# Performance work log

Measured on AMD Instinct MI355X. Metric: run time of the kernel, lower is better.

The kernel has to match this reference:

```python
import jax, jax.numpy as jnp
import numpy as np

B, S, D, H = 2, 2048, 1024, 16
Dh = D // H

def setup_inputs() -> dict:
    key = jax.random.key(0)
    ks = jax.random.split(key, 11)
    def lin(k, fan_in):
        bound = 1.0 / np.sqrt(fan_in)
        kw, kb = jax.random.split(k)
        W = jax.random.uniform(kw, (D, D), jnp.float32, -bound, bound)
        b = jax.random.uniform(kb, (D,), jnp.float32, -bound, bound)
        return W, b
    Wq, bq = lin(ks[0], D)
    Wk, bk = lin(ks[1], D)
    Wv, bv = lin(ks[2], D)
    Wo, bo = lin(ks[3], D)
    Q = jax.random.normal(ks[4], (B, S, D), jnp.float32)
    K = jax.random.normal(ks[5], (B, S, D), jnp.float32)
    V = jax.random.normal(ks[6], (B, S, D), jnp.float32)
    return {"Q": Q, "K": K, "V": V, "Wq": Wq, "bq": bq, "Wk": Wk, "bk": bk,
            "Wv": Wv, "bv": bv, "Wo": Wo, "bo": bo}

def _split_heads(x):
    # [B,S,D] -> [B,H,S,Dh]
    b, s, _ = x.shape
    return x.reshape(b, s, H, Dh).transpose(0, 2, 1, 3)

def reference(Q, K, V, Wq, bq, Wk, bk, Wv, bv, Wo, bo):
    q = _split_heads(Q @ Wq.T + bq)
    k = _split_heads(K @ Wk.T + bk)
    v = _split_heads(V @ Wv.T + bv)
    scores = jnp.einsum('bhqd,bhkd->bhqk', q, k) / jnp.sqrt(jnp.float32(Dh))
    attn = jax.nn.softmax(scores, axis=-1)
    out = jnp.einsum('bhqk,bhkd->bhqd', attn, v)  # [B,H,S,Dh]
    out = out.transpose(0, 2, 1, 3).reshape(Q.shape[0], Q.shape[1], D)
    return out @ Wo.T + bo
```

## Files before the change

### kernel.cpp

```cpp
#include <hip/hip_runtime.h>

#define SEQ 2048
#define DMODEL 1024
#define NH 16
#define DH 64

typedef __attribute__((ext_vector_type(8))) short bf16x8;
typedef __attribute__((ext_vector_type(4))) short bf16x4;
typedef __attribute__((ext_vector_type(4))) float floatx4;
typedef __attribute__((ext_vector_type(4))) unsigned short u16x4;
typedef unsigned short u16;
typedef unsigned int u32;

typedef const void __attribute__((address_space(1)))* as1cvp;
typedef void __attribute__((address_space(3)))* as3vp;

__device__ __forceinline__ void glds16(const void* g, void* l) {
    __builtin_amdgcn_global_load_lds((as1cvp)g, (as3vp)l, 16, 0, 0);
}

__device__ __forceinline__ u16 f2bf(float f) {
    union { u32 u; float f; } v; v.f = f;
    return (u16)((v.u + 0x8000u) >> 16);
}

__device__ __forceinline__ u32 pk2(float a, float b) {
    union { u32 u; float f; } x, y; x.f = a; y.f = b;
    u32 xr = x.u + 0x8000u, yr = y.u + 0x8000u;
#if __has_builtin(__builtin_amdgcn_perm)
    return __builtin_amdgcn_perm(yr, xr, 0x07060302u);
#else
    return (xr >> 16) | (yr & 0xffff0000u);
#endif
}

__device__ __forceinline__ float ex2(float x) {
#if __has_builtin(__builtin_amdgcn_exp2f)
    return __builtin_amdgcn_exp2f(x);
#else
    float r; asm("v_exp_f32 %0, %1" : "=v"(r) : "v"(x)); return r;
#endif
}

__device__ __forceinline__ floatx4 mfma16(bf16x4 a, bf16x4 b, floatx4 c) {
#if __has_builtin(__builtin_amdgcn_mfma_f32_16x16x16bf16_1k)
    return __builtin_amdgcn_mfma_f32_16x16x16bf16_1k(a, b, c, 0, 0, 0);
#else
    asm volatile("v_mfma_f32_16x16x16_bf16 %0, %1, %2, %0" : "+v"(c) : "v"(a), "v"(b));
    return c;
#endif
}

__device__ __forceinline__ uint4 cvt8(const float* __restrict__ p) {
    float4 a = *(const float4*)p;
    float4 b = *(const float4*)(p + 4);
    uint4 q;
    q.x = pk2(a.x, a.y); q.y = pk2(a.z, a.w);
    q.z = pk2(b.x, b.y); q.w = pk2(b.z, b.w);
    return q;
}

#define QSCALE 0.18033688011112042f

__global__ __launch_bounds__(256) void cvt_all(
    const float* __restrict__ Q, const float* __restrict__ K, const float* __restrict__ V,
    const float* __restrict__ W0, const float* __restrict__ W1,
    const float* __restrict__ W2, const float* __restrict__ W3,
    u16* __restrict__ Qb, u16* __restrict__ Kb, u16* __restrict__ Vb,
    u16* __restrict__ Wb)
{
    const int y = blockIdx.y;
    const float* src; u16* dst;
    if (y == 0)      { src = Q;  dst = Qb; }
    else if (y == 1) { src = K;  dst = Kb; }
    else if (y == 2) { src = V;  dst = Vb; }
    else {
        if (blockIdx.x >= 512) return;
        src = (y == 3) ? W0 : (y == 4) ? W1 : (y == 5) ? W2 : W3;
        dst = Wb + (size_t)(y - 3) * 1048576;
    }
    size_t i = ((size_t)blockIdx.x * 256 + threadIdx.x) * 8;
    *(uint4*)(dst + i) = cvt8(src + i);
}

__global__ __launch_bounds__(256) void cvt_w(
    const float* __restrict__ W0, const float* __restrict__ W1,
    const float* __restrict__ W2, const float* __restrict__ W3,
    u16* __restrict__ out)
{
    const float* src = (blockIdx.y == 0) ? W0 : (blockIdx.y == 1) ? W1
                     : (blockIdx.y == 2) ? W2 : W3;
    size_t i = ((size_t)blockIdx.x * 256 + threadIdx.x) * 8;
    *(uint4*)(out + (size_t)blockIdx.y * 1048576 + i) = cvt8(src + i);
}

__device__ __forceinline__ void qkv_store(
    int z, u16* __restrict__ outp, int rowg, int col, floatx4 a4, float bv, float sc)
{
    union { u32 w[2]; u16 h[4]; u16x4 v4; } pk;
    pk.w[0] = pk2((a4[0] + bv) * sc, (a4[1] + bv) * sc);
    pk.w[1] = pk2((a4[2] + bv) * sc, (a4[3] + bv) * sc);
    int b = rowg >> 11, s = rowg & 2047, h = col >> 6, d = col & 63;
    if (z < 2) {
#pragma unroll
        for (int r = 0; r < 4; r++)
            outp[((size_t)(b * NH + h) * SEQ + s + r) * DH + d] = pk.h[r];
    } else {
        *(u16x4*)(outp + ((size_t)(b * NH + h) * DH + d) * SEQ + s) = pk.v4;
    }
}

__global__ __launch_bounds__(256) void gemm_qkv_bb(
    const u16* __restrict__ Qb, const u16* __restrict__ Kb, const u16* __restrict__ Vb,
    const u16* __restrict__ Wb,
    const float* __restrict__ b0, const float* __restrict__ b1, const float* __restrict__ b2,
    u16* __restrict__ qo, u16* __restrict__ ko, u16* __restrict__ vto)
{
    __shared__ __align__(16) u16 As[3][4096];
    __shared__ __align__(16) u16 Bs[3][4096];
    const int tid = threadIdx.x, l = tid & 63, w = tid >> 6;
    const int lm = l & 15, quad = l >> 4;
    const int wr = (w >> 1) * 64, wc = (w & 1) * 64;
    const int bm = blockIdx.y * 128, bn = blockIdx.x * 128;
    const int z = blockIdx.z;
    const u16* A      = (z == 0) ? Qb : (z == 1) ? Kb : Vb;
    const u16* W      = Wb + (size_t)z * 1048576;
    const float* bias = (z == 0) ? b0 : (z == 1) ? b1 : b2;

    const int srow = tid >> 2, scol = (tid & 3) * 8;

    floatx4 acc[4][4];
#pragma unroll
    for (int i = 0; i < 4; i++)
#pragma unroll
        for (int j = 0; j < 4; j++) acc[i][j] = (floatx4){0.f, 0.f, 0.f, 0.f};

#define QKV_STAGE(I, NB) do { \
        const int kt_ = (I) * 32; \
        glds16(A + (size_t)(bm + srow) * DMODEL + kt_ + scol, As[NB] + w * 512); \
        glds16(A + (size_t)(bm + 64 + srow) * DMODEL + kt_ + scol, As[NB] + 2048 + w * 512); \
        glds16(W + (size_t)(bn + srow) * DMODEL + kt_ + scol, Bs[NB] + w * 512); \
        glds16(W + (size_t)(bn + 64 + srow) * DMODEL + kt_ + scol, Bs[NB] + 2048 + w * 512); \
    } while (0)

    QKV_STAGE(0, 0);
    QKV_STAGE(1, 1);
    asm volatile("s_waitcnt vmcnt(4)" ::: "memory");
    __builtin_amdgcn_s_barrier();

    int cur = 0, nx = 2;
    for (int i = 0; i < 32; i++) {
        bf16x8 af[4], bfr[4];
#pragma unroll
        for (int mi = 0; mi < 4; mi++)
            af[mi] = *(const bf16x8*)(As[cur] + (wr + mi * 16 + lm) * 32 + quad * 8);
#pragma unroll
        for (int ni = 0; ni < 4; ni++)
            bfr[ni] = *(const bf16x8*)(Bs[cur] + (wc + ni * 16 + lm) * 32 + quad * 8);
#pragma unroll
        for (int mi = 0; mi < 4; mi++)
#pragma unroll
            for (int ni = 0; ni < 4; ni++)
                acc[mi][ni] = __builtin_amdgcn_mfma_f32_16x16x32_bf16(
                    af[mi], bfr[ni], acc[mi][ni], 0, 0, 0);

        if (i + 2 < 32) {
            QKV_STAGE(i + 2, nx);
            asm volatile("s_waitcnt vmcnt(4)" ::: "memory");
            __builtin_amdgcn_s_barrier();
        } else if (i + 1 < 32) {
            asm volatile("s_waitcnt vmcnt(0)" ::: "memory");
            __builtin_amdgcn_s_barrier();
        }
        cur = (cur == 2) ? 0 : cur + 1;
        nx  = (nx == 2) ? 0 : nx + 1;
    }
#undef QKV_STAGE

    const float sc = (z == 0) ? QSCALE : 1.0f;
    u16* outp = (z == 0) ? qo : (z == 1) ? ko : vto;
#pragma unroll
    for (int ni = 0; ni < 4; ni++) {
        int col = bn + wc + ni * 16 + lm;
        float bv = bias[col];
#pragma unroll
        for (int mi = 0; mi < 4; mi++)
            qkv_store(z, outp, bm + wr + mi * 16 + quad * 4, col, acc[mi][ni], bv, sc);
    }
}

template<bool WBF>
__global__ __launch_bounds__(256) void gemm_qkv(
    const float* __restrict__ Qf, const float* __restrict__ Kf, const float* __restrict__ Vf,
    const void* __restrict__ W0, const void* __restrict__ W1, const void* __restrict__ W2,
    const float* __restrict__ b0, const float* __restrict__ b1, const float* __restrict__ b2,
    u16* __restrict__ qo, u16* __restrict__ ko, u16* __restrict__ vto)
{
    __shared__ __align__(16) u16 As[128 * 32];
    __shared__ __align__(16) u16 Bs[128 * 32];
    const int tid = threadIdx.x, l = tid & 63, w = tid >> 6;
    const int lm = l & 15, quad = l >> 4;
    const int wr = (w >> 1) * 64, wc = (w & 1) * 64;
    const int bm = blockIdx.y * 128, bn = blockIdx.x * 128;
    const int z = blockIdx.z;
    const float* A    = (z == 0) ? Qf : (z == 1) ? Kf : Vf;
    const void* Wp    = (z == 0) ? W0 : (z == 1) ? W1 : W2;
    const float* bias = (z == 0) ? b0 : (z == 1) ? b1 : b2;

    floatx4 acc[4][4];
#pragma unroll
    for (int i = 0; i < 4; i++)
#pragma unroll
        for (int j = 0; j < 4; j++) acc[i][j] = (floatx4){0.f, 0.f, 0.f, 0.f};

    for (int kt = 0; kt < DMODEL; kt += 32) {
        __syncthreads();
#pragma unroll
        for (int j = 0; j < 2; j++) {
            int ch = j * 256 + tid, row = ch >> 2, c = ch & 3;
            *(uint4*)(As + ch * 8) = cvt8(A + (size_t)(bm + row) * DMODEL + kt + c * 8);
        }
        if (WBF) {
            const u16* Wc = (const u16*)Wp;
            glds16(Wc + (size_t)(bn + (tid >> 2)) * DMODEL + kt + (tid & 3) * 8, Bs + w * 512);
            glds16(Wc + (size_t)(bn + 64 + (tid >> 2)) * DMODEL + kt + (tid & 3) * 8, Bs + 2048 + w * 512);
        } else {
            const float* Wf = (const float*)Wp;
#pragma unroll
            for (int j = 0; j < 2; j++) {
                int ch = j * 256 + tid, row = ch >> 2, c = ch & 3;
                *(uint4*)(Bs + ch * 8) = cvt8(Wf + (size_t)(bn + row) * DMODEL + kt + c * 8);
            }
        }
        __syncthreads();

        bf16x8 af[4], bfr[4];
#pragma unroll
        for (int mi = 0; mi < 4; mi++)
            af[mi] = *(const bf16x8*)(As + (wr + mi * 16 + lm) * 32 + quad * 8);
#pragma unroll
        for (int ni = 0; ni < 4; ni++)
            bfr[ni] = *(const bf16x8*)(Bs + (wc + ni * 16 + lm) * 32 + quad * 8);
#pragma unroll
        for (int mi = 0; mi < 4; mi++)
#pragma unroll
            for (int ni = 0; ni < 4; ni++)
                acc[mi][ni] = __builtin_amdgcn_mfma_f32_16x16x32_bf16(
                    af[mi], bfr[ni], acc[mi][ni], 0, 0, 0);
    }

    const float sc = (z == 0) ? QSCALE : 1.0f;
    u16* outp = (z == 0) ? qo : (z == 1) ? ko : vto;
#pragma unroll
    for (int ni = 0; ni < 4; ni++) {
        int col = bn + wc + ni * 16 + lm;
        float bv = bias[col];
#pragma unroll
        for (int mi = 0; mi < 4; mi++)
            qkv_store(z, outp, bm + wr + mi * 16 + quad * 4, col, acc[mi][ni], bv, sc);
    }
}

__global__ __launch_bounds__(256) void gemm_o_p(
    const u16* __restrict__ A, const u16* __restrict__ W,
    const float* __restrict__ bias, float* __restrict__ out)
{
    __shared__ __align__(16) u16 As[3][4096];
    __shared__ __align__(16) u16 Bs[3][2048];
    const int tid = threadIdx.x, l = tid & 63, w = tid >> 6;
    const int lm = l & 15, quad = l >> 4;
    const int bm = blockIdx.y * 128, bn = blockIdx.x * 64;

    floatx4 acc[2][4];
#pragma unroll
    for (int i = 0; i < 2; i++)
#pragma unroll
        for (int j = 0; j < 4; j++) acc[i][j] = (floatx4){0.f, 0.f, 0.f, 0.f};

#define O_STAGE(I, NB) do { \
        const int kt_ = (I) * 32; \
        glds16(A + (size_t)(bm + (tid >> 2)) * DMODEL + kt_ + (tid & 3) * 8, As[NB] + w * 512); \
        glds16(A + (size_t)(bm + 64 + (tid >> 2)) * DMODEL + kt_ + (tid & 3) * 8, As[NB] + 2048 + w * 512); \
        glds16(W + (size_t)(bn + (tid >> 2)) * DMODEL + kt_ + (tid & 3) * 8, Bs[NB] + w * 512); \
    } while (0)

    O_STAGE(0, 0);
    O_STAGE(1, 1);
    asm volatile("s_waitcnt vmcnt(3)" ::: "memory");
    __builtin_amdgcn_s_barrier();

    int cur = 0, nx = 2;
    for (int i = 0; i < 32; i++) {
        bf16x8 af[2], bfr[4];
#pragma unroll
        for (int mi = 0; mi < 2; mi++)
            af[mi] = *(const bf16x8*)(As[cur] + (w * 32 + mi * 16 + lm) * 32 + quad * 8);
#pragma unroll
        for (int ni = 0; ni < 4; ni++)
            bfr[ni] = *(const bf16x8*)(Bs[cur] + (ni * 16 + lm) * 32 + quad * 8);
#pragma unroll
        for (int mi = 0; mi < 2; mi++)
#pragma unroll
            for (int ni = 0; ni < 4; ni++)
                acc[mi][ni] = __builtin_amdgcn_mfma_f32_16x16x32_bf16(
                    af[mi], bfr[ni], acc[mi][ni], 0, 0, 0);

        if (i + 2 < 32) {
            O_STAGE(i + 2, nx);
            asm volatile("s_waitcnt vmcnt(3)" ::: "memory");
            __builtin_amdgcn_s_barrier();
        } else if (i + 1 < 32) {
            asm volatile("s_waitcnt vmcnt(0)" ::: "memory");
            __builtin_amdgcn_s_barrier();
        }
        cur = (cur == 2) ? 0 : cur + 1;
        nx  = (nx == 2) ? 0 : nx + 1;
    }
#undef O_STAGE

#pragma unroll
    for (int ni = 0; ni < 4; ni++) {
        int col = bn + ni * 16 + lm;
        float bv = bias[col];
#pragma unroll
        for (int mi = 0; mi < 2; mi++) {
#pragma unroll
            for (int r = 0; r < 4; r++) {
                int rowg = bm + w * 32 + mi * 16 + quad * 4 + r;
                out[(size_t)rowg * DMODEL + col] = acc[mi][ni][r] + bv;
            }
        }
    }
}

template<bool WBF>
__global__ __launch_bounds__(256) void gemm_o(
    const u16* __restrict__ A, const void* __restrict__ Wp,
    const float* __restrict__ bias, float* __restrict__ out)
{
    __shared__ __align__(16) u16 As[128 * 32];
    __shared__ __align__(16) u16 Bs[64 * 32];
    const int tid = threadIdx.x, l = tid & 63, w = tid >> 6;
    const int lm = l & 15, quad = l >> 4;
    const int bm = blockIdx.y * 128, bn = blockIdx.x * 64;

    floatx4 acc[2][4];
#pragma unroll
    for (int i = 0; i < 2; i++)
#pragma unroll
        for (int j = 0; j < 4; j++) acc[i][j] = (floatx4){0.f, 0.f, 0.f, 0.f};

    for (int kt = 0; kt < DMODEL; kt += 32) {
        __syncthreads();
        glds16(A + (size_t)(bm + (tid >> 2)) * DMODEL + kt + (tid & 3) * 8, As + w * 512);
        glds16(A + (size_t)(bm + 64 + (tid >> 2)) * DMODEL + kt + (tid & 3) * 8, As + 2048 + w * 512);
        if (WBF) {
            glds16((const u16*)Wp + (size_t)(bn + (tid >> 2)) * DMODEL + kt + (tid & 3) * 8, Bs + w * 512);
        } else {
            *(uint4*)(Bs + tid * 8) =
                cvt8((const float*)Wp + (size_t)(bn + (tid >> 2)) * DMODEL + kt + (tid & 3) * 8);
        }
        __syncthreads();

        bf16x8 af[2], bfr[4];
#pragma unroll
        for (int mi = 0; mi < 2; mi++)
            af[mi] = *(const bf16x8*)(As + (w * 32 + mi * 16 + lm) * 32 + quad * 8);
#pragma unroll
        for (int ni = 0; ni < 4; ni++)
            bfr[ni] = *(const bf16x8*)(Bs + (ni * 16 + lm) * 32 + quad * 8);
#pragma unroll
        for (int mi = 0; mi < 2; mi++)
#pragma unroll
            for (int ni = 0; ni < 4; ni++)
                acc[mi][ni] = __builtin_amdgcn_mfma_f32_16x16x32_bf16(
                    af[mi], bfr[ni], acc[mi][ni], 0, 0, 0);
    }

#pragma unroll
    for (int ni = 0; ni < 4; ni++) {
        int col = bn + ni * 16 + lm;
        float bv = bias[col];
#pragma unroll
        for (int mi = 0; mi < 2; mi++) {
#pragma unroll
            for (int r = 0; r < 4; r++) {
                int rowg = bm + w * 32 + mi * 16 + quad * 4 + r;
                out[(size_t)rowg * DMODEL + col] = acc[mi][ni][r] + bv;
            }
        }
    }
}

#define SP 72
#define TS (64 * SP)
#define BUFSZ (4 * TS)
__global__ __launch_bounds__(256, 2) void attn_kernel(
    const u16* __restrict__ q, const u16* __restrict__ k,
    const u16* __restrict__ vt, u16* __restrict__ out)
{
    __shared__ __align__(16) u16 smem[2 * BUFSZ];
    const int tid = threadIdx.x, l = tid & 63, w = tid >> 6;
    const int lm = l & 15, quad = l >> 4;
    const int qt = blockIdx.x, bh = blockIdx.y;
    const int b = bh >> 4, h = bh & 15;
    const int rg = w & 1, half = w >> 1;

    bf16x8 qf[4][2];
#pragma unroll
    for (int nt = 0; nt < 4; nt++) {
        int row = qt * 128 + rg * 64 + nt * 16 + lm;
        const u16* qp = q + ((size_t)bh * SEQ + row) * DH;
        qf[nt][0] = *(const bf16x8*)(qp + quad * 8);
        qf[nt][1] = *(const bf16x8*)(qp + 32 + quad * 8);
    }

    floatx4 O[4][4];
#pragma unroll
    for (int dt = 0; dt < 4; dt++)
#pragma unroll
        for (int nt = 0; nt < 4; nt++) O[dt][nt] = (floatx4){0.f, 0.f, 0.f, 0.f};
    floatx4 Ol[4];
#pragma unroll
    for (int nt = 0; nt < 4; nt++) Ol[nt] = (floatx4){0.f, 0.f, 0.f, 0.f};

    const bf16x4 onesb = {(short)0x3F80, (short)0x3F80, (short)0x3F80, (short)0x3F80};

    const int srow = tid >> 2, sc4 = tid & 3;
    const u16* kbase = k + (size_t)bh * SEQ * DH;
    const u16* vbase = vt + (size_t)bh * DH * SEQ;

    uint4 kA0, kA1, kB0, kB1, vA0, vA1, vB0, vB1;
#define LOADT(T) do { \
        const u16* kgA = kbase + (size_t)((T) * 64 + srow) * DH + sc4 * 16; \
        const u16* kgB = kbase + (size_t)(1024 + (T) * 64 + srow) * DH + sc4 * 16; \
        kA0 = *(const uint4*)kgA;       kA1 = *(const uint4*)(kgA + 8); \
        kB0 = *(const uint4*)kgB;       kB1 = *(const uint4*)(kgB + 8); \
        const u16* vgA = vbase + (size_t)srow * SEQ + (T) * 64 + sc4 * 16; \
        const u16* vgB = vgA + 1024; \
        vA0 = *(const uint4*)vgA;       vA1 = *(const uint4*)(vgA + 8); \
        vB0 = *(const uint4*)vgB;       vB1 = *(const uint4*)(vgB + 8); \
    } while (0)
#define WRBUF(BUF) do { \
        u16* K0 = smem + (BUF) * BUFSZ; \
        u16* K1 = K0 + TS; \
        u16* V0 = K0 + 2 * TS; \
        u16* V1 = K0 + 3 * TS; \
        *(uint4*)(K0 + srow * SP + sc4 * 16)     = kA0; \
        *(uint4*)(K0 + srow * SP + sc4 * 16 + 8) = kA1; \
        *(uint4*)(K1 + srow * SP + sc4 * 16)     = kB0; \
        *(uint4*)(K1 + srow * SP + sc4 * 16 + 8) = kB1; \
        *(uint2*)(V0 + srow * SP + 0 * 16 + sc4 * 4) = make_uint2(vA0.x, vA0.y); \
        *(uint2*)(V0 + srow * SP + 1 * 16 + sc4 * 4) = make_uint2(vA0.z, vA0.w); \
        *(uint2*)(V0 + srow * SP + 2 * 16 + sc4 * 4) = make_uint2(vA1.x, vA1.y); \
        *(uint2*)(V0 + srow * SP + 3 * 16 + sc4 * 4) = make_uint2(vA1.z, vA1.w); \
        *(uint2*)(V1 + srow * SP + 0 * 16 + sc4 * 4) = make_uint2(vB0.x, vB0.y); \
        *(uint2*)(V1 + srow * SP + 1 * 16 + sc4 * 4) = make_uint2(vB0.z, vB0.w); \
        *(uint2*)(V1 + srow * SP + 2 * 16 + sc4 * 4) = make_uint2(vB1.x, vB1.y); \
        *(uint2*)(V1 + srow * SP + 3 * 16 + sc4 * 4) = make_uint2(vB1.z, vB1.w); \
    } while (0)

    LOADT(0);
    WRBUF(0);
    LOADT(1);
    asm volatile("s_waitcnt lgkmcnt(0)" ::: "memory");
    __builtin_amdgcn_s_barrier();

    for (int t = 0; t < 16; t++) {
        const int cur = t & 1;
        const u16* Kh = smem + cur * BUFSZ + half * TS;
        const u16* Vh = smem + cur * BUFSZ + (2 + half) * TS;

        floatx4 Sc[4][4];
        __builtin_amdgcn_s_setprio(1);
#pragma unroll
        for (int mt = 0; mt < 4; mt++) {
            bf16x8 ka0 = *(const bf16x8*)(Kh + (mt * 16 + lm) * SP + quad * 8);
            bf16x8 ka1 = *(const bf16x8*)(Kh + (mt * 16 + lm) * SP + 32 + quad * 8);
#pragma unroll
            for (int nt = 0; nt < 4; nt++) {
                floatx4 c = (floatx4){0.f, 0.f, 0.f, 0.f};
                c = __builtin_amdgcn_mfma_f32_16x16x32_bf16(ka0, qf[nt][0], c, 0, 0, 0);
                c = __builtin_amdgcn_mfma_f32_16x16x32_bf16(ka1, qf[nt][1], c, 0, 0, 0);
                Sc[mt][nt] = c;
            }
        }
        __builtin_amdgcn_s_setprio(0);

        if (t + 1 < 16) {
            asm volatile("s_waitcnt vmcnt(0)" ::: "memory");
            WRBUF(cur ^ 1);
            if (t + 2 < 16) LOADT(t + 2);
        }

        bf16x4 pb[4][4];
#pragma unroll
        for (int mt = 0; mt < 4; mt++) {
#pragma unroll
            for (int nt = 0; nt < 4; nt++) {
#pragma unroll
                for (int r = 0; r < 4; r++) Sc[mt][nt][r] = ex2(Sc[mt][nt][r]);
                union { u32 w2[2]; bf16x4 v; } pku;
                pku.w2[0] = pk2(Sc[mt][nt][0], Sc[mt][nt][1]);
                pku.w2[1] = pk2(Sc[mt][nt][2], Sc[mt][nt][3]);
                pb[mt][nt] = pku.v;
            }
        }

        __builtin_amdgcn_s_setprio(1);
#pragma unroll
        for (int nt = 0; nt < 4; nt++) {
            Ol[nt] = mfma16(onesb, pb[0][nt], Ol[nt]);
            Ol[nt] = mfma16(onesb, pb[1][nt], Ol[nt]);
            Ol[nt] = mfma16(onesb, pb[2][nt], Ol[nt]);
            Ol[nt] = mfma16(onesb, pb[3][nt], Ol[nt]);
        }

#pragma unroll
        for (int dt = 0; dt < 4; dt++) {
            const u16* vp = Vh + (dt * 16 + lm) * SP + quad * 16;
            bf16x8 v8a = *(const bf16x8*)vp;
            bf16x8 v8b = *(const bf16x8*)(vp + 8);
            bf16x4 va0 = __builtin_shufflevector(v8a, v8a, 0, 1, 2, 3);
            bf16x4 va1 = __builtin_shufflevector(v8a, v8a, 4, 5, 6, 7);
            bf16x4 va2 = __builtin_shufflevector(v8b, v8b, 0, 1, 2, 3);
            bf16x4 va3 = __builtin_shufflevector(v8b, v8b, 4, 5, 6, 7);
#pragma unroll
            for (int nt = 0; nt < 4; nt++) {
                O[dt][nt] = mfma16(va0, pb[0][nt], O[dt][nt]);
                O[dt][nt] = mfma16(va1, pb[1][nt], O[dt][nt]);
                O[dt][nt] = mfma16(va2, pb[2][nt], O[dt][nt]);
                O[dt][nt] = mfma16(va3, pb[3][nt], O[dt][nt]);
            }
        }
        __builtin_amdgcn_s_setprio(0);

        asm volatile("s_waitcnt lgkmcnt(0)" ::: "memory");
        __builtin_amdgcn_s_barrier();
    }
#undef LOADT
#undef WRBUF

    float* obuf  = (float*)smem;
    float* mlbuf = (float*)smem + 8704;
    if (w >= 2) {
        float* ob = obuf + (rg * 64 + l) * 68;
        float* ml = mlbuf + (rg * 64 + l) * 5;
#pragma unroll
        for (int nt = 0; nt < 4; nt++) {
#pragma unroll
            for (int dt = 0; dt < 4; dt++)
                *(floatx4*)(ob + nt * 16 + dt * 4) = O[dt][nt];
            ml[nt] = Ol[nt][0];
        }
    }
    __syncthreads();
    if (w < 2) {
        float* ob = obuf + (rg * 64 + l) * 68;
        float* ml = mlbuf + (rg * 64 + l) * 5;
#pragma unroll
        for (int nt = 0; nt < 4; nt++) {
            float lB = ml[nt];
            float inv = 1.0f / (Ol[nt][0] + lB);
            int s = qt * 128 + rg * 64 + nt * 16 + lm;
            u16* op = out + ((size_t)b * SEQ + s) * DMODEL + h * DH;
#pragma unroll
            for (int dt = 0; dt < 4; dt++) {
                floatx4 Ob = *(const floatx4*)(ob + nt * 16 + dt * 4);
                union { u32 w2[2]; u16x4 v; } pku;
                pku.w2[0] = pk2((O[dt][nt][0] + Ob[0]) * inv,
                                (O[dt][nt][1] + Ob[1]) * inv);
                pku.w2[1] = pk2((O[dt][nt][2] + Ob[2]) * inv,
                                (O[dt][nt][3] + Ob[3]) * inv);
                *(u16x4*)(op + dt * 16 + quad * 4) = pku.v;
            }
        }
    }
}

extern "C" void kernel_launch(void* const* d_in, const int* in_sizes, int n_in,
                              void* d_out, int out_size, void* d_ws, size_t ws_size,
                              hipStream_t stream) {
    (void)in_sizes; (void)n_in; (void)out_size;
    const float* Q  = (const float*)d_in[0];
    const float* K  = (const float*)d_in[1];
    const float* V  = (const float*)d_in[2];
    const float* Wq = (const float*)d_in[3];
    const float* bq = (const float*)d_in[4];
    const float* Wk = (const float*)d_in[5];
    const float* bk = (const float*)d_in[6];
    const float* Wv = (const float*)d_in[7];
    const float* bv = (const float*)d_in[8];
    const float* Wo = (const float*)d_in[9];
    const float* bo = (const float*)d_in[10];

    const size_t NEL = (size_t)2 * NH * SEQ * DH;
    u16* base = (u16*)d_ws;
    dim3 bb(256);
    dim3 ab(256);

    if (ws_size >= 8 * NEL * 2) {
        u16* Qb   = base;
        u16* Kb   = Qb + NEL;
        u16* Vb   = Kb + NEL;
        u16* Wb   = Vb + NEL;
        u16* qws  = Wb + NEL;
        u16* kws  = qws + NEL;
        u16* vtws = kws + NEL;
        u16* aws  = vtws + NEL;
        cvt_all<<<dim3(2048, 7), bb, 0, stream>>>(Q, K, V, Wq, Wk, Wv, Wo, Qb, Kb, Vb, Wb);
        gemm_qkv_bb<<<dim3(8, 32, 3), bb, 0, stream>>>(
            Qb, Kb, Vb, Wb, bq, bk, bv, qws, kws, vtws);
        attn_kernel<<<dim3(SEQ / 128, 2 * NH), ab, 0, stream>>>(qws, kws, vtws, aws);
        gemm_o_p<<<dim3(16, 32), bb, 0, stream>>>(aws, Wb + 3145728, bo, (float*)d_out);
    } else if (ws_size >= 5 * NEL * 2) {
        u16* Wb = base;
        u16* qws = base + NEL; u16* kws = qws + NEL; u16* vtws = kws + NEL; u16* aws = vtws + NEL;
        cvt_w<<<dim3(512, 4), bb, 0, stream>>>(Wq, Wk, Wv, Wo, Wb);
        gemm_qkv<true><<<dim3(8, 32, 3), bb, 0, stream>>>(
            Q, K, V, Wb, Wb + 1048576, Wb + 2097152, bq, bk, bv, qws, kws, vtws);
        attn_kernel<<<dim3(SEQ / 128, 2 * NH), ab, 0, stream>>>(qws, kws, vtws, aws);
        gemm_o_p<<<dim3(16, 32), bb, 0, stream>>>(aws, Wb + 3145728, bo, (float*)d_out);
    } else {
        u16* qws = base; u16* kws = qws + NEL; u16* vtws = kws + NEL; u16* aws = vtws + NEL;
        gemm_qkv<false><<<dim3(8, 32, 3), bb, 0, stream>>>(
            Q, K, V, Wq, Wk, Wv, bq, bk, bv, qws, kws, vtws);
        attn_kernel<<<dim3(SEQ / 128, 2 * NH), ab, 0, stream>>>(qws, kws, vtws, aws);
        gemm_o<false><<<dim3(16, 32), bb, 0, stream>>>(aws, Wo, bo, (float*)d_out);
    }
}
```

Measured before the change: 220.8 us.

## Use 16x16x32 bf16 MFMA for PV and row-sum via permuted K layout

Replaces the 16x16x16 MFMAs in the P·V and row-sum accumulation with 16x16x32 MFMAs, halving the instruction count. K rows are stored to LDS under a permutation so that two adjacent score tiles pack into one 8-wide bf16 operand that lines up with contiguous V columns. V stores become plain 16-byte writes and its fragment loads no longer need splitting. Correctness depends on the row permutation exactly matching the MFMA k-index ordering.

New measurement: 218.7 us. No clear change (-0.9%).

```diff
diff --git a/kernel.cpp b/kernel.cpp
--- a/kernel.cpp
+++ b/kernel.cpp
@@ -42,13 +42,8 @@
 #endif
 }
 
-__device__ __forceinline__ floatx4 mfma16(bf16x4 a, bf16x4 b, floatx4 c) {
-#if __has_builtin(__builtin_amdgcn_mfma_f32_16x16x16bf16_1k)
-    return __builtin_amdgcn_mfma_f32_16x16x16bf16_1k(a, b, c, 0, 0, 0);
-#else
-    asm volatile("v_mfma_f32_16x16x16_bf16 %0, %1, %2, %0" : "+v"(c) : "v"(a), "v"(b));
-    return c;
-#endif
+__device__ __forceinline__ floatx4 mfma32(bf16x8 a, bf16x8 b, floatx4 c) {
+    return __builtin_amdgcn_mfma_f32_16x16x32_bf16(a, b, c, 0, 0, 0);
 }
 
 __device__ __forceinline__ uint4 cvt8(const float* __restrict__ p) {
@@ -424,9 +419,11 @@
 #pragma unroll
     for (int nt = 0; nt < 4; nt++) Ol[nt] = (floatx4){0.f, 0.f, 0.f, 0.f};
 
-    const bf16x4 onesb = {(short)0x3F80, (short)0x3F80, (short)0x3F80, (short)0x3F80};
+    const bf16x8 ones8 = {(short)0x3F80, (short)0x3F80, (short)0x3F80, (short)0x3F80,
+                          (short)0x3F80, (short)0x3F80, (short)0x3F80, (short)0x3F80};
 
     const int srow = tid >> 2, sc4 = tid & 3;
+    const int prow = (srow & 32) | ((srow & 4) << 2) | ((srow & 24) >> 1) | (srow & 3);
     const u16* kbase = k + (size_t)bh * SEQ * DH;
     const u16* vbase = vt + (size_t)bh * DH * SEQ;
 
@@ -446,18 +443,14 @@
         u16* K1 = K0 + TS; \
         u16* V0 = K0 + 2 * TS; \
         u16* V1 = K0 + 3 * TS; \
-        *(uint4*)(K0 + srow * SP + sc4 * 16)     = kA0; \
-        *(uint4*)(K0 + srow * SP + sc4 * 16 + 8) = kA1; \
-        *(uint4*)(K1 + srow * SP + sc4 * 16)     = kB0; \
-        *(uint4*)(K1 + srow * SP + sc4 * 16 + 8) = kB1; \
-        *(uint2*)(V0 + srow * SP + 0 * 16 + sc4 * 4) = make_uint2(vA0.x, vA0.y); \
-        *(uint2*)(V0 + srow * SP + 1 * 16 + sc4 * 4) = make_uint2(vA0.z, vA0.w); \
-        *(uint2*)(V0 + srow * SP + 2 * 16 + sc4 * 4) = make_uint2(vA1.x, vA1.y); \
-        *(uint2*)(V0 + srow * SP + 3 * 16 + sc4 * 4) = make_uint2(vA1.z, vA1.w); \
-        *(uint2*)(V1 + srow * SP + 0 * 16 + sc4 * 4) = make_uint2(vB0.x, vB0.y); \
-        *(uint2*)(V1 + srow * SP + 1 * 16 + sc4 * 4) = make_uint2(vB0.z, vB0.w); \
-        *(uint2*)(V1 + srow * SP + 2 * 16 + sc4 * 4) = make_uint2(vB1.x, vB1.y); \
-        *(uint2*)(V1 + srow * SP + 3 * 16 + sc4 * 4) = make_uint2(vB1.z, vB1.w); \
+        *(uint4*)(K0 + prow * SP + sc4 * 16)     = kA0; \
+        *(uint4*)(K0 + prow * SP + sc4 * 16 + 8) = kA1; \
+        *(uint4*)(K1 + prow * SP + sc4 * 16)     = kB0; \
+        *(uint4*)(K1 + prow * SP + sc4 * 16 + 8) = kB1; \
+        *(uint4*)(V0 + srow * SP + sc4 * 16)     = vA0; \
+        *(uint4*)(V0 + srow * SP + sc4 * 16 + 8) = vA1; \
+        *(uint4*)(V1 + srow * SP + sc4 * 16)     = vB0; \
+        *(uint4*)(V1 + srow * SP + sc4 * 16 + 8) = vB1; \
     } while (0)
 
     LOADT(0);
@@ -474,15 +467,15 @@
         floatx4 Sc[4][4];
         __builtin_amdgcn_s_setprio(1);
 #pragma unroll
-        for (int mt = 0; mt < 4; mt++) {
-            bf16x8 ka0 = *(const bf16x8*)(Kh + (mt * 16 + lm) * SP + quad * 8);
-            bf16x8 ka1 = *(const bf16x8*)(Kh + (mt * 16 + lm) * SP + 32 + quad * 8);
+        for (int sub = 0; sub < 4; sub++) {
+            bf16x8 ka0 = *(const bf16x8*)(Kh + (sub * 16 + lm) * SP + quad * 8);
+            bf16x8 ka1 = *(const bf16x8*)(Kh + (sub * 16 + lm) * SP + 32 + quad * 8);
 #pragma unroll
             for (int nt = 0; nt < 4; nt++) {
                 floatx4 c = (floatx4){0.f, 0.f, 0.f, 0.f};
-                c = __builtin_amdgcn_mfma_f32_16x16x32_bf16(ka0, qf[nt][0], c, 0, 0, 0);
-                c = __builtin_amdgcn_mfma_f32_16x16x32_bf16(ka1, qf[nt][1], c, 0, 0, 0);
-                Sc[mt][nt] = c;
+                c = mfma32(ka0, qf[nt][0], c);
+                c = mfma32(ka1, qf[nt][1], c);
+                Sc[sub][nt] = c;
             }
         }
         __builtin_amdgcn_s_setprio(0);
@@ -493,44 +486,37 @@
             if (t + 2 < 16) LOADT(t + 2);
         }
 
-        bf16x4 pb[4][4];
-#pragma unroll
-        for (int mt = 0; mt < 4; mt++) {
+        bf16x8 pbm[2][4];
+#pragma unroll
+        for (int p = 0; p < 2; p++)
 #pragma unroll
             for (int nt = 0; nt < 4; nt++) {
-#pragma unroll
-                for (int r = 0; r < 4; r++) Sc[mt][nt][r] = ex2(Sc[mt][nt][r]);
-                union { u32 w2[2]; bf16x4 v; } pku;
-                pku.w2[0] = pk2(Sc[mt][nt][0], Sc[mt][nt][1]);
-                pku.w2[1] = pk2(Sc[mt][nt][2], Sc[mt][nt][3]);
-                pb[mt][nt] = pku.v;
+                floatx4 sa = Sc[p * 2][nt], sb = Sc[p * 2 + 1][nt];
+#pragma unroll
+                for (int r = 0; r < 4; r++) { sa[r] = ex2(sa[r]); sb[r] = ex2(sb[r]); }
+                union { u32 w4[4]; bf16x8 v; } pku;
+                pku.w4[0] = pk2(sa[0], sa[1]);
+                pku.w4[1] = pk2(sa[2], sa[3]);
+                pku.w4[2] = pk2(sb[0], sb[1]);
+                pku.w4[3] = pk2(sb[2], sb[3]);
+                pbm[p][nt] = pku.v;
             }
-        }
 
         __builtin_amdgcn_s_setprio(1);
 #pragma unroll
         for (int nt = 0; nt < 4; nt++) {
-            Ol[nt] = mfma16(onesb, pb[0][nt], Ol[nt]);
-            Ol[nt] = mfma16(onesb, pb[1][nt], Ol[nt]);
-            Ol[nt] = mfma16(onesb, pb[2][nt], Ol[nt]);
-            Ol[nt] = mfma16(onesb, pb[3][nt], Ol[nt]);
+            Ol[nt] = mfma32(ones8, pbm[0][nt], Ol[nt]);
+            Ol[nt] = mfma32(ones8, pbm[1][nt], Ol[nt]);
         }
 
 #pragma unroll
         for (int dt = 0; dt < 4; dt++) {
-            const u16* vp = Vh + (dt * 16 + lm) * SP + quad * 16;
-            bf16x8 v8a = *(const bf16x8*)vp;
-            bf16x8 v8b = *(const bf16x8*)(vp + 8);
-            bf16x4 va0 = __builtin_shufflevector(v8a, v8a, 0, 1, 2, 3);
-            bf16x4 va1 = __builtin_shufflevector(v8a, v8a, 4, 5, 6, 7);
-            bf16x4 va2 = __builtin_shufflevector(v8b, v8b, 0, 1, 2, 3);
-            bf16x4 va3 = __builtin_shufflevector(v8b, v8b, 4, 5, 6, 7);
+            bf16x8 va0 = *(const bf16x8*)(Vh + (dt * 16 + lm) * SP + quad * 8);
+            bf16x8 va1 = *(const bf16x8*)(Vh + (dt * 16 + lm) * SP + 32 + quad * 8);
 #pragma unroll
             for (int nt = 0; nt < 4; nt++) {
-                O[dt][nt] = mfma16(va0, pb[0][nt], O[dt][nt]);
-                O[dt][nt] = mfma16(va1, pb[1][nt], O[dt][nt]);
-                O[dt][nt] = mfma16(va2, pb[2][nt], O[dt][nt]);
-                O[dt][nt] = mfma16(va3, pb[3][nt], O[dt][nt]);
+                O[dt][nt] = mfma32(va0, pbm[0][nt], O[dt][nt]);
+                O[dt][nt] = mfma32(va1, pbm[1][nt], O[dt][nt]);
             }
         }
         __builtin_amdgcn_s_setprio(0);
```
